# Kernel optimization log

Measured on AMD Instinct MI355X. Metric: run time of the kernel, lower is better.

Reference implementation:

```python
import jax, jax.numpy as jnp
import numpy as np

N = 2_000_000


def _make_boxes(key, n):
    # valid boxes: x2 > x1, y2 > y1 (widths/heights positive for the log)
    k1, k2 = jax.random.split(key)
    xy1 = jax.random.uniform(k1, (1, n, 2), dtype=jnp.float32) * 500.0
    wh = jax.random.uniform(k2, (1, n, 2), dtype=jnp.float32) * 100.0 + 1.0
    return jnp.concatenate([xy1, xy1 + wh], axis=-1)  # [1,n,4]


def setup_inputs() -> dict:
    key = jax.random.key(0)
    k1, k2, k3, k4 = jax.random.split(key, 4)
    gt_boxes = _make_boxes(k1, N)
    roi_boxes = _make_boxes(k2, N)
    # gt_rois: [1,N,5], only cols :4 used; pad a class col
    gt_rois = jnp.concatenate([gt_boxes, jnp.zeros((1, N, 1), jnp.float32)], axis=-1)
    # rois: [1,N,5], col 0 is batch index, cols 1:5 are the box
    rois = jnp.concatenate([jnp.zeros((1, N, 1), jnp.float32), roi_boxes], axis=-1)
    labels = jax.random.randint(k3, (N,), 0, 21, dtype=jnp.int64)
    means = jnp.array([0.0, 0.0, 0.0, 0.0], jnp.float32)
    stds = jnp.array([0.1, 0.1, 0.2, 0.2], jnp.float32)
    inside_w = jnp.array([1.0, 1.0, 1.0, 1.0], jnp.float32)
    return {"gt_rois": gt_rois, "rois": rois, "labels": labels,
            "means": means, "stds": stds, "inside_w": inside_w}


def _bbox_transform_batch(ex_rois, gt_rois):
    ex_w = ex_rois[..., 2] - ex_rois[..., 0] + 1.0
    ex_h = ex_rois[..., 3] - ex_rois[..., 1] + 1.0
    ex_cx = ex_rois[..., 0] + 0.5 * ex_w
    ex_cy = ex_rois[..., 1] + 0.5 * ex_h
    gt_w = gt_rois[..., 2] - gt_rois[..., 0] + 1.0
    gt_h = gt_rois[..., 3] - gt_rois[..., 1] + 1.0
    gt_cx = gt_rois[..., 0] + 0.5 * gt_w
    gt_cy = gt_rois[..., 1] + 0.5 * gt_h
    dx = (gt_cx - ex_cx) / ex_w
    dy = (gt_cy - ex_cy) / ex_h
    dw = jnp.log(gt_w / ex_w)
    dh = jnp.log(gt_h / ex_h)
    return jnp.stack([dx, dy, dw, dh], axis=-1)  # [B,N,4]


def reference(gt_rois, rois, labels, means, stds, inside_w):
    targets = _bbox_transform_batch(rois[:, :, 1:5], gt_rois[:, :, :4])  # [1,N,4]
    targets = (targets - means) / stds  # BBOX_NORMALIZE_TARGETS_PRECOMPUTED=True
    pos = (labels > 0)[None, :, None]  # [1,N,1]
    bbox_targets = jnp.where(pos, targets, 0.0)
    bbox_inside_weights = jnp.where(pos, inside_w, 0.0)  # broadcast [4] -> [1,N,4]
    bbox_outside_weights = (bbox_inside_weights > 0).astype(targets.dtype)
    return bbox_targets, bbox_inside_weights, bbox_outside_weights
```

## Files before the change

### kernel.cpp

```cpp
#include <hip/hip_runtime.h>
#include <hip/hip_bf16.h>


__global__ __launch_bounds__(256) void rcnn_target_kernel(
    const float* __restrict__ gt_rois,
    const float* __restrict__ rois,
    const int*   __restrict__ labels,
    const float* __restrict__ means,
    const float* __restrict__ stds,
    const float* __restrict__ inside_w,
    float* __restrict__ out,
    int n)
{
    const float m0 = means[0], m1 = means[1], m2 = means[2], m3 = means[3];
    const float rs0 = 1.0f / stds[0], rs1 = 1.0f / stds[1];
    const float rs2 = 1.0f / stds[2], rs3 = 1.0f / stds[3];
    const float iw0 = inside_w[0], iw1 = inside_w[1];
    const float iw2 = inside_w[2], iw3 = inside_w[3];

    float4* __restrict__ out_t  = reinterpret_cast<float4*>(out);
    float4* __restrict__ out_wi = reinterpret_cast<float4*>(out + 4ull * (size_t)n);
    float4* __restrict__ out_wo = reinterpret_cast<float4*>(out + 8ull * (size_t)n);

    const int stride = gridDim.x * blockDim.x;
    for (int i = blockIdx.x * blockDim.x + threadIdx.x; i < n; i += stride) {
        const float* g = gt_rois + (size_t)i * 5;
        const float* r = rois    + (size_t)i * 5 + 1;

        const float gx1 = g[0], gy1 = g[1], gx2 = g[2], gy2 = g[3];
        const float ex1 = r[0], ey1 = r[1], ex2 = r[2], ey2 = r[3];

        const float ew  = ex2 - ex1 + 1.0f;
        const float eh  = ey2 - ey1 + 1.0f;
        const float ecx = ex1 + 0.5f * ew;
        const float ecy = ey1 + 0.5f * eh;
        const float gw  = gx2 - gx1 + 1.0f;
        const float gh  = gy2 - gy1 + 1.0f;
        const float gcx = gx1 + 0.5f * gw;
        const float gcy = gy1 + 0.5f * gh;

        const float dx = (gcx - ecx) / ew;
        const float dy = (gcy - ecy) / eh;
        const float dw = logf(gw / ew);
        const float dh = logf(gh / eh);

        const bool pos = labels[i] > 0;

        float4 t;
        t.x = pos ? (dx - m0) * rs0 : 0.0f;
        t.y = pos ? (dy - m1) * rs1 : 0.0f;
        t.z = pos ? (dw - m2) * rs2 : 0.0f;
        t.w = pos ? (dh - m3) * rs3 : 0.0f;

        float4 wi;
        wi.x = pos ? iw0 : 0.0f;
        wi.y = pos ? iw1 : 0.0f;
        wi.z = pos ? iw2 : 0.0f;
        wi.w = pos ? iw3 : 0.0f;

        float4 wo;
        wo.x = (wi.x > 0.0f) ? 1.0f : 0.0f;
        wo.y = (wi.y > 0.0f) ? 1.0f : 0.0f;
        wo.z = (wi.z > 0.0f) ? 1.0f : 0.0f;
        wo.w = (wi.w > 0.0f) ? 1.0f : 0.0f;

        out_t[i]  = t;
        out_wi[i] = wi;
        out_wo[i] = wo;
    }
}

extern "C" void kernel_launch(void* const* d_in, const int* in_sizes, int n_in,
                              void* d_out, int out_size, void* d_ws, size_t ws_size,
                              hipStream_t stream)
{
    const float* gt_rois  = (const float*)d_in[0];
    const float* rois     = (const float*)d_in[1];
    const int*   labels   = (const int*)d_in[2];
    const float* means    = (const float*)d_in[3];
    const float* stds     = (const float*)d_in[4];
    const float* inside_w = (const float*)d_in[5];
    float* out = (float*)d_out;

    const int n = in_sizes[2];

    const int block = 256;
    int grid = (n + block - 1) / block;
    if (grid > 2048) grid = 2048;

    rcnn_target_kernel<<<grid, block, 0, stream>>>(
        gt_rois, rois, labels, means, stds, inside_w, out, n);
}
```

Before: 33.20 us.

## Stage stride-5 ROI inputs through shared memory with coalesced float4 loads

Each block now loads its contiguous chunk of gt_rois and rois into LDS with float4 vector loads, then each thread reads its 5-float record from shared memory. This replaces strided scalar global loads (stride 20 bytes) with fully coalesced vector loads. The grid-stride loop is also dropped in favour of one element per thread with a full grid, which adds a block barrier and LDS traffic per block.

```diff
diff --git a/kernel.cpp b/kernel.cpp
--- a/kernel.cpp
+++ b/kernel.cpp
@@ -2,7 +2,9 @@
 #include <hip/hip_bf16.h>
 
 
-__global__ __launch_bounds__(256) void rcnn_target_kernel(
+#define BLOCK 256
+
+__global__ __launch_bounds__(BLOCK) void rcnn_target_kernel(
     const float* __restrict__ gt_rois,
     const float* __restrict__ rois,
     const int*   __restrict__ labels,
@@ -12,62 +14,88 @@
     float* __restrict__ out,
     int n)
 {
+    __shared__ float sg[BLOCK * 5];
+    __shared__ float sr[BLOCK * 5];
+
+    const int base = blockIdx.x * BLOCK;
+    const int rem  = min(BLOCK, n - base);
+    const int nflt = 5 * rem;
+    const int nvec = nflt >> 2;
+
+    const float4* __restrict__ g4 = reinterpret_cast<const float4*>(gt_rois + (size_t)base * 5);
+    const float4* __restrict__ r4 = reinterpret_cast<const float4*>(rois    + (size_t)base * 5);
+    float4* __restrict__ sg4 = reinterpret_cast<float4*>(sg);
+    float4* __restrict__ sr4 = reinterpret_cast<float4*>(sr);
+
+    for (int idx = threadIdx.x; idx < nvec; idx += BLOCK) {
+        sg4[idx] = g4[idx];
+        sr4[idx] = r4[idx];
+    }
+    if (threadIdx.x == 0) {
+        for (int f = nvec * 4; f < nflt; ++f) {
+            sg[f] = gt_rois[(size_t)base * 5 + f];
+            sr[f] = rois[(size_t)base * 5 + f];
+        }
+    }
+    __syncthreads();
+
+    const int t = threadIdx.x;
+    const int i = base + t;
+    if (i >= n) return;
+
     const float m0 = means[0], m1 = means[1], m2 = means[2], m3 = means[3];
     const float rs0 = 1.0f / stds[0], rs1 = 1.0f / stds[1];
     const float rs2 = 1.0f / stds[2], rs3 = 1.0f / stds[3];
     const float iw0 = inside_w[0], iw1 = inside_w[1];
     const float iw2 = inside_w[2], iw3 = inside_w[3];
 
+    const float* g = sg + 5 * t;
+    const float* r = sr + 5 * t + 1;
+
+    const float gx1 = g[0], gy1 = g[1], gx2 = g[2], gy2 = g[3];
+    const float ex1 = r[0], ey1 = r[1], ex2 = r[2], ey2 = r[3];
+
+    const float ew  = ex2 - ex1 + 1.0f;
+    const float eh  = ey2 - ey1 + 1.0f;
+    const float ecx = ex1 + 0.5f * ew;
+    const float ecy = ey1 + 0.5f * eh;
+    const float gw  = gx2 - gx1 + 1.0f;
+    const float gh  = gy2 - gy1 + 1.0f;
+    const float gcx = gx1 + 0.5f * gw;
+    const float gcy = gy1 + 0.5f * gh;
+
+    const float dx = (gcx - ecx) / ew;
+    const float dy = (gcy - ecy) / eh;
+    const float dw = logf(gw / ew);
+    const float dh = logf(gh / eh);
+
+    const bool pos = labels[i] > 0;
+
+    float4 tg;
+    tg.x = pos ? (dx - m0) * rs0 : 0.0f;
+    tg.y = pos ? (dy - m1) * rs1 : 0.0f;
+    tg.z = pos ? (dw - m2) * rs2 : 0.0f;
+    tg.w = pos ? (dh - m3) * rs3 : 0.0f;
+
+    float4 wi;
+    wi.x = pos ? iw0 : 0.0f;
+    wi.y = pos ? iw1 : 0.0f;
+    wi.z = pos ? iw2 : 0.0f;
+    wi.w = pos ? iw3 : 0.0f;
+
+    float4 wo;
+    wo.x = (wi.x > 0.0f) ? 1.0f : 0.0f;
+    wo.y = (wi.y > 0.0f) ? 1.0f : 0.0f;
+    wo.z = (wi.z > 0.0f) ? 1.0f : 0.0f;
+    wo.w = (wi.w > 0.0f) ? 1.0f : 0.0f;
+
     float4* __restrict__ out_t  = reinterpret_cast<float4*>(out);
     float4* __restrict__ out_wi = reinterpret_cast<float4*>(out + 4ull * (size_t)n);
     float4* __restrict__ out_wo = reinterpret_cast<float4*>(out + 8ull * (size_t)n);
 
-    const int stride = gridDim.x * blockDim.x;
-    for (int i = blockIdx.x * blockDim.x + threadIdx.x; i < n; i += stride) {
-        const float* g = gt_rois + (size_t)i * 5;
-        const float* r = rois    + (size_t)i * 5 + 1;
-
-        const float gx1 = g[0], gy1 = g[1], gx2 = g[2], gy2 = g[3];
-        const float ex1 = r[0], ey1 = r[1], ex2 = r[2], ey2 = r[3];
-
-        const float ew  = ex2 - ex1 + 1.0f;
-        const float eh  = ey2 - ey1 + 1.0f;
-        const float ecx = ex1 + 0.5f * ew;
-        const float ecy = ey1 + 0.5f * eh;
-        const float gw  = gx2 - gx1 + 1.0f;
-        const float gh  = gy2 - gy1 + 1.0f;
-        const float gcx = gx1 + 0.5f * gw;
-        const float gcy = gy1 + 0.5f * gh;
-
-        const float dx = (gcx - ecx) / ew;
-        const float dy = (gcy - ecy) / eh;
-        const float dw = logf(gw / ew);
-        const float dh = logf(gh / eh);
-
-        const bool pos = labels[i] > 0;
-
-        float4 t;
-        t.x = pos ? (dx - m0) * rs0 : 0.0f;
-        t.y = pos ? (dy - m1) * rs1 : 0.0f;
-        t.z = pos ? (dw - m2) * rs2 : 0.0f;
-        t.w = pos ? (dh - m3) * rs3 : 0.0f;
-
-        float4 wi;
-        wi.x = pos ? iw0 : 0.0f;
-        wi.y = pos ? iw1 : 0.0f;
-        wi.z = pos ? iw2 : 0.0f;
-        wi.w = pos ? iw3 : 0.0f;
-
-        float4 wo;
-        wo.x = (wi.x > 0.0f) ? 1.0f : 0.0f;
-        wo.y = (wi.y > 0.0f) ? 1.0f : 0.0f;
-        wo.z = (wi.z > 0.0f) ? 1.0f : 0.0f;
-        wo.w = (wi.w > 0.0f) ? 1.0f : 0.0f;
-
-        out_t[i]  = t;
-        out_wi[i] = wi;
-        out_wo[i] = wo;
-    }
+    out_t[i]  = tg;
+    out_wi[i] = wi;
+    out_wo[i] = wo;
 }
 
 extern "C" void kernel_launch(void* const* d_in, const int* in_sizes, int n_in,
@@ -84,10 +112,7 @@
 
     const int n = in_sizes[2];
 
-    const int block = 256;
-    int grid = (n + block - 1) / block;
-    if (grid > 2048) grid = 2048;
-
-    rcnn_target_kernel<<<grid, block, 0, stream>>>(
+    const int grid = (n + BLOCK - 1) / BLOCK;
+    rcnn_target_kernel<<<grid, BLOCK, 0, stream>>>(
         gt_rois, rois, labels, means, stds, inside_w, out, n);
 }
```

Result: no change. 32.67 us (-1.6%).
